# Performance work log

Hardware: AMD Instinct MI355X
Metric: run time of the kernel (lower is better)

The kernel has to match this reference:

```python
import jax, jax.numpy as jnp
import numpy as np

N, E, B = 80000, 480000, 800  # nodes, edges, graphs
H, C = 4, 64                  # attention heads, per-head channels

def gelu(x):
    return jax.nn.gelu(x, approximate=False)

def setup_inputs() -> dict:
    key = jax.random.key(0)
    ks = jax.random.split(key, 40)
    nrm = lambda k, shp, s=0.1: jax.random.normal(k, shp, jnp.float32) * s
    inp = {
        'x': jax.random.normal(ks[0], (N, 21), jnp.float32),
        'edge_index': jax.random.randint(ks[1], (2, E), 0, N, dtype=jnp.int32),
        'batch_idx': jnp.sort(jax.random.randint(ks[2], (N,), 0, B, dtype=jnp.int32)),
        'rnafm': jax.random.normal(ks[3], (B, 640), jnp.float32),
        'hand_feat': jax.random.normal(ks[4], (B, 40), jnp.float32),
        # GATConv params: lin weight [H*C, in], att_src/att_dst [H, C], bias [C]
        'g1_W': nrm(ks[5], (H * C, 21)), 'g1_as': nrm(ks[6], (H, C)), 'g1_ad': nrm(ks[7], (H, C)), 'g1_b': nrm(ks[8], (C,)),
        'g2_W': nrm(ks[9], (H * C, C)), 'g2_as': nrm(ks[10], (H, C)), 'g2_ad': nrm(ks[11], (H, C)), 'g2_b': nrm(ks[12], (C,)),
        'g3_W': nrm(ks[13], (H * C, C)), 'g3_as': nrm(ks[14], (H, C)), 'g3_ad': nrm(ks[15], (H, C)), 'g3_b': nrm(ks[16], (C,)),
        'pool_W': nrm(ks[17], (1, C)), 'pool_b': nrm(ks[18], (1,)),
        'e1_W': nrm(ks[19], (256, 744)), 'e1_b': nrm(ks[20], (256,)),
        'ln_g': jnp.ones((256,), jnp.float32), 'ln_b': jnp.zeros((256,), jnp.float32),
        'e2_W': nrm(ks[21], (128, 256)), 'e2_b': nrm(ks[22], (128,)),
        'bin_W': nrm(ks[23], (1, 128)), 'bin_b': nrm(ks[24], (1,)),
        'ad1_W': nrm(ks[25], (5, 32, 128)), 'ad1_b': nrm(ks[26], (5, 32)),
        'ad2_W': nrm(ks[27], (5, 1, 32)), 'ad2_b': nrm(ks[28], (5, 1)),
        'c1_W': nrm(ks[29], (64, 128)), 'c1_b': nrm(ks[30], (64,)),
        'c2_W': nrm(ks[31], (6, 64)), 'c2_b': nrm(ks[32], (6,)),
    }
    return inp


def reference(x, edge_index, batch_idx, rnafm, hand_feat,
              g1_W, g1_as, g1_ad, g1_b,
              g2_W, g2_as, g2_ad, g2_b,
              g3_W, g3_as, g3_ad, g3_b,
              pool_W, pool_b, e1_W, e1_b, ln_g, ln_b, e2_W, e2_b,
              bin_W, bin_b, ad1_W, ad1_b, ad2_W, ad2_b, c1_W, c1_b, c2_W, c2_b):
    n = x.shape[0]
    # PyG GATConv default: add self loops
    loops = jnp.arange(n, dtype=edge_index.dtype)
    ei = jnp.concatenate([edge_index, jnp.stack([loops, loops])], axis=1)
    src, dst = ei[0], ei[1]

    def gat(h_in, W, a_s, a_d, b):
        h = (h_in @ W.T).reshape(n, H, C)              # [N,H,C]
        s = (h * a_s[None]).sum(-1)                    # [N,H] att_src . h
        d = (h * a_d[None]).sum(-1)                    # [N,H]
        e = jax.nn.leaky_relu(s[src] + d[dst], 0.2)    # [E',H]
        m = jax.ops.segment_max(e, dst, num_segments=n)
        ex = jnp.exp(e - m[dst])                       # segment softmax (stable)
        z = jax.ops.segment_sum(ex, dst, num_segments=n)
        alpha = ex / z[dst]                            # [E',H]
        out = jax.ops.segment_sum(h[src] * alpha[:, :, None], dst, num_segments=n)
        return out.mean(axis=1) + b                    # concat=False -> mean heads

    h = gelu(gat(x, g1_W, g1_as, g1_ad, g1_b))
    h = gelu(gat(h, g2_W, g2_as, g2_ad, g2_b))
    h = gelu(gat(h, g3_W, g3_as, g3_ad, g3_b))

    # attention-weighted pooling; softmax over ALL nodes (dim=0), as in source
    attn = jax.nn.softmax(h @ pool_W.T + pool_b, axis=0)   # [N,1]
    pooled = jax.ops.segment_sum(h * attn, batch_idx, num_segments=B)  # [B,64]

    fused = jnp.concatenate([pooled, rnafm, hand_feat], axis=-1)       # [B,744]
    z1 = gelu(fused @ e1_W.T + e1_b)
    mu = z1.mean(-1, keepdims=True)
    var = ((z1 - mu) ** 2).mean(-1, keepdims=True)
    z1 = (z1 - mu) / jnp.sqrt(var + 1e-5) * ln_g + ln_b
    shared = gelu(z1 @ e2_W.T + e2_b)                      # [B,128]

    binary = (shared @ bin_W.T + bin_b)[:, 0]              # [B]
    h1 = gelu(jnp.einsum('bd,ehd->ebh', shared, ad1_W) + ad1_b[:, None, :])
    per = jnp.einsum('ebh,eh->eb', h1, ad2_W[:, 0, :]) + ad2_b  # [5,B]
    cls = gelu(shared @ c1_W.T + c1_b) @ c2_W.T + c2_b     # [B,6]
    return binary, per, cls
```

## Files before the change

kernel.cpp:

```cpp
#include <hip/hip_runtime.h>
#include <hip/hip_bf16.h>
#include <math.h>

constexpr int N_NODES = 80000;
constexpr int N_EDGES = 480000;
constexpr int N_B     = 800;
constexpr int PADDEG  = 64;

typedef __attribute__((ext_vector_type(8))) short bf16x8;
typedef __attribute__((ext_vector_type(4))) float f32x4;

__device__ __forceinline__ float gelu_exact(float x) {
    return 0.5f * x * (1.0f + erff(x * 0.70710678118654752f));
}
__device__ __forceinline__ float lrelu(float v) {
    return v > 0.f ? v : 0.2f * v;
}
__device__ __forceinline__ unsigned short f2bf(float f) {
    unsigned u = __float_as_uint(f);
    unsigned r = u + 0x7FFFu + ((u >> 16) & 1u);
    return (unsigned short)(r >> 16);
}
__device__ __forceinline__ float bf2f(unsigned short h) {
    return __uint_as_float(((unsigned)h) << 16);
}

template<int IN_DIM>
__launch_bounds__(256, 2)
__global__ void gat_transform(const float* __restrict__ xin,
                              const float* __restrict__ W,
                              const float* __restrict__ aS,
                              const float* __restrict__ aD,
                              unsigned short* __restrict__ hfull,
                              float* __restrict__ sArr,
                              float* __restrict__ dArr) {
    constexpr int K  = (IN_DIM + 31) & ~31;
    constexpr int KS = K / 32;
    constexpr int KP = K + 8;
    __shared__ __align__(16) unsigned short Wb[256 * KP];
    __shared__ __align__(16) unsigned short xs[32 * KP];

    const int tid = threadIdx.x;
    const int lane = tid & 63, w = tid >> 6;

    for (int idx = tid; idx < 256 * K; idx += 256) {
        int c = idx / K, k = idx - c * K;
        Wb[c * KP + k] = (k < IN_DIM) ? f2bf(W[c * IN_DIM + k]) : (unsigned short)0;
    }
    __syncthreads();

    bf16x8 bfrag[4][KS];
    float asv[4], adv[4];
#pragma unroll
    for (int t = 0; t < 4; ++t) {
        const int ch = w * 64 + t * 16 + (lane & 15);
#pragma unroll
        for (int s = 0; s < KS; ++s)
            bfrag[t][s] = *reinterpret_cast<const bf16x8*>(&Wb[ch * KP + s * 32 + (lane >> 4) * 8]);
        asv[t] = aS[ch];
        adv[t] = aD[ch];
    }

    const int ntiles = N_NODES / 32;
    for (int tile = blockIdx.x; tile < ntiles; tile += gridDim.x) {
        const int n0 = tile * 32;
        __syncthreads();
        for (int idx = tid; idx < 32 * K; idx += 256) {
            int r = idx / K, k = idx - r * K;
            xs[r * KP + k] = (k < IN_DIM) ? f2bf(xin[(size_t)(n0 + r) * IN_DIM + k])
                                          : (unsigned short)0;
        }
        __syncthreads();

        f32x4 acc[2][4];
#pragma unroll
        for (int m = 0; m < 2; ++m) {
            bf16x8 afrag[KS];
#pragma unroll
            for (int s = 0; s < KS; ++s)
                afrag[s] = *reinterpret_cast<const bf16x8*>(
                    &xs[(m * 16 + (lane & 15)) * KP + s * 32 + (lane >> 4) * 8]);
#pragma unroll
            for (int t = 0; t < 4; ++t) {
                f32x4 a = {0.f, 0.f, 0.f, 0.f};
#pragma unroll
                for (int s = 0; s < KS; ++s)
                    a = __builtin_amdgcn_mfma_f32_16x16x32_bf16(afrag[s], bfrag[t][s], a, 0, 0, 0);
                acc[m][t] = a;
            }
        }

#pragma unroll
        for (int m = 0; m < 2; ++m) {
            float sv[4] = {0, 0, 0, 0}, dv[4] = {0, 0, 0, 0};
#pragma unroll
            for (int t = 0; t < 4; ++t) {
                const int ch = w * 64 + t * 16 + (lane & 15);
#pragma unroll
                for (int j = 0; j < 4; ++j) {
                    float hv = acc[m][t][j];
                    int node = n0 + m * 16 + (lane >> 4) * 4 + j;
                    hfull[(size_t)node * 256 + ch] = f2bf(hv);
                    sv[j] += hv * asv[t];
                    dv[j] += hv * adv[t];
                }
            }
#pragma unroll
            for (int j = 0; j < 4; ++j) {
                sv[j] += __shfl_xor(sv[j], 1, 64); dv[j] += __shfl_xor(dv[j], 1, 64);
                sv[j] += __shfl_xor(sv[j], 2, 64); dv[j] += __shfl_xor(dv[j], 2, 64);
                sv[j] += __shfl_xor(sv[j], 4, 64); dv[j] += __shfl_xor(dv[j], 4, 64);
                sv[j] += __shfl_xor(sv[j], 8, 64); dv[j] += __shfl_xor(dv[j], 8, 64);
                if ((lane & 15) == 0) {
                    int node = n0 + m * 16 + (lane >> 4) * 4 + j;
                    sArr[node * 4 + w] = sv[j];
                    dArr[node * 4 + w] = dv[j];
                }
            }
        }
    }
}

__global__ void csr_scatter_pad(const int* __restrict__ ei,
                                int* __restrict__ cnt, int* __restrict__ csrc) {
    int e = blockIdx.x * 256 + threadIdx.x;
    if (e >= N_EDGES) return;
    int src = ei[e], dst = ei[N_EDGES + e];
    int slot = atomicAdd(&cnt[dst], 1);
    csrc[(size_t)dst * PADDEG + slot] = src;
}

template<bool POOL>
__launch_bounds__(256)
__global__ void gat_gather(const int* __restrict__ cnt, const int* __restrict__ csrc,
                           const float* __restrict__ sArr, const float* __restrict__ dArr,
                           const unsigned short* __restrict__ hfull,
                           const float* __restrict__ bias,
                           const float* __restrict__ poolW, const float* __restrict__ poolB,
                           float* __restrict__ xout,
                           float* __restrict__ logit, float* __restrict__ pmax) {
    constexpr int CAP = PADDEG;
    __shared__ float qbuf[4][2][CAP * 4];
    __shared__ int   sbuf[4][2][CAP];
    __shared__ float xbuf[4][2][64];
    __shared__ float red[8];

    const int wid = threadIdx.x >> 6;
    const int lane = threadIdx.x & 63;
    const int nl = lane >> 5;
    const int sub = lane & 31;
    const int n = blockIdx.x * 8 + wid * 2 + nl;

    const int jb = n * PADDEG;
    const int deg = cnt[n];

    const int hh = sub & 3;
    const int slot = sub >> 2;
    const float dv = dArr[n * 4 + hh];
    const float lself = lrelu(sArr[n * 4 + hh] + dv);
    float m = lself;

    for (int base = 0; base < deg; base += 8) {
        int s = base + slot;
        float lg = -INFINITY;
        if (s < deg) {
            int src = csrc[jb + s];
            lg = lrelu(sArr[src * 4 + hh] + dv);
            qbuf[wid][nl][s * 4 + hh] = lg;
            if (hh == 0) sbuf[wid][nl][s] = src;
        }
        m = fmaxf(m, lg);
    }
    m = fmaxf(m, __shfl_xor(m, 4, 64));
    m = fmaxf(m, __shfl_xor(m, 8, 64));
    m = fmaxf(m, __shfl_xor(m, 16, 64));
    __threadfence_block();

    float zp = 0.f;
    for (int base = 0; base < deg; base += 8) {
        int s = base + slot;
        if (s < deg) {
            float q = expf(qbuf[wid][nl][s * 4 + hh] - m);
            qbuf[wid][nl][s * 4 + hh] = q;
            zp += q;
        }
    }
    const float qself = expf(lself - m);
    zp += __shfl_xor(zp, 4, 64);
    zp += __shfl_xor(zp, 8, 64);
    zp += __shfl_xor(zp, 16, 64);
    const float inv = 0.25f / (zp + qself);
    __threadfence_block();

    const int h = sub >> 3;
    const int c8 = sub * 8;
    const int bl = (lane & 32) + h;
    const float inv_g = __shfl(inv, bl, 64);
    const float qs_g  = __shfl(qself, bl, 64);

#define LOADU4(S) (*reinterpret_cast<const uint4*>(&hfull[(size_t)(unsigned)(S) * 256 + c8]))
#define UNPK_FMA(A, Q, U) { \
    A[0] = fmaf((Q), __uint_as_float((U).x << 16),          A[0]); \
    A[1] = fmaf((Q), __uint_as_float((U).x & 0xFFFF0000u),  A[1]); \
    A[2] = fmaf((Q), __uint_as_float((U).y << 16),          A[2]); \
    A[3] = fmaf((Q), __uint_as_float((U).y & 0xFFFF0000u),  A[3]); \
    A[4] = fmaf((Q), __uint_as_float((U).z << 16),          A[4]); \
    A[5] = fmaf((Q), __uint_as_float((U).z & 0xFFFF0000u),  A[5]); \
    A[6] = fmaf((Q), __uint_as_float((U).w << 16),          A[6]); \
    A[7] = fmaf((Q), __uint_as_float((U).w & 0xFFFF0000u),  A[7]); }

    float accA[8] = {0, 0, 0, 0, 0, 0, 0, 0};
    float accB[8] = {0, 0, 0, 0, 0, 0, 0, 0};
    {
        uint4 us = LOADU4(n);
        UNPK_FMA(accA, qs_g, us);
    }
    int s = 0;
    for (; s + 1 < deg; s += 2) {
        int s0 = sbuf[wid][nl][s], s1 = sbuf[wid][nl][s + 1];
        float q0 = qbuf[wid][nl][s * 4 + h];
        float q1 = qbuf[wid][nl][(s + 1) * 4 + h];
        uint4 u0 = LOADU4(s0);
        uint4 u1 = LOADU4(s1);
        UNPK_FMA(accA, q0, u0);
        UNPK_FMA(accB, q1, u1);
    }
    if (s < deg) {
        int s0 = sbuf[wid][nl][s];
        float q0 = qbuf[wid][nl][s * 4 + h];
        uint4 u0 = LOADU4(s0);
        UNPK_FMA(accA, q0, u0);
    }
#undef UNPK_FMA
#undef LOADU4

    float acc[8];
#pragma unroll
    for (int j = 0; j < 8; ++j) acc[j] = (accA[j] + accB[j]) * inv_g;

#pragma unroll
    for (int j = 0; j < 8; ++j) {
        acc[j] += __shfl_xor(acc[j], 8, 64);
        acc[j] += __shfl_xor(acc[j], 16, 64);
    }

    {
        float w0 = (h == 0) ? acc[0] : (h == 1) ? acc[2] : (h == 2) ? acc[4] : acc[6];
        float w1 = (h == 0) ? acc[1] : (h == 1) ? acc[3] : (h == 2) ? acc[5] : acc[7];
        const int rc = (sub & 7) * 8 + h * 2;
        xbuf[wid][nl][rc]     = w0;
        xbuf[wid][nl][rc + 1] = w1;
    }
    __threadfence_block();

    const int c2 = sub * 2;
    float o0 = gelu_exact(xbuf[wid][nl][c2]     + bias[c2]);
    float o1 = gelu_exact(xbuf[wid][nl][c2 + 1] + bias[c2 + 1]);
    *reinterpret_cast<float2*>(&xout[(size_t)n * 64 + c2]) = make_float2(o0, o1);

    if (POOL) {
        float p = o0 * poolW[c2] + o1 * poolW[c2 + 1];
#pragma unroll
        for (int of = 1; of < 32; of <<= 1) p += __shfl_xor(p, of, 64);
        float lg = p + poolB[0];
        if (sub == 0) {
            logit[n] = lg;
            red[wid * 2 + nl] = lg;
        }
        __syncthreads();
        if (threadIdx.x == 0) {
            float mm = red[0];
#pragma unroll
            for (int i = 1; i < 8; ++i) mm = fmaxf(mm, red[i]);
            pmax[blockIdx.x] = mm;
        }
    }
}

__global__ void reduce_max(const float* __restrict__ pmax, int n,
                           float* __restrict__ gmax) {
    __shared__ float red[256];
    float m = -INFINITY;
    for (int i = threadIdx.x; i < n; i += 256) m = fmaxf(m, pmax[i]);
    red[threadIdx.x] = m;
    __syncthreads();
    for (int s = 128; s > 0; s >>= 1) {
        if (threadIdx.x < s) red[threadIdx.x] = fmaxf(red[threadIdx.x], red[threadIdx.x + s]);
        __syncthreads();
    }
    if (threadIdx.x == 0) *gmax = red[0];
}

__global__ void seg_bounds(const int* __restrict__ batch, int* __restrict__ start) {
    int n = blockIdx.x * 256 + threadIdx.x;
    if (n >= N_NODES) return;
    int b1 = batch[n];
    int b0 = (n == 0) ? -1 : batch[n - 1];
    for (int b = b0 + 1; b <= b1; ++b) start[b] = n;
    if (n == N_NODES - 1)
        for (int b = b1 + 1; b <= N_B; ++b) start[b] = N_NODES;
}

__global__ void pool_graph(const float* __restrict__ h3,
                           const float* __restrict__ logit,
                           const float* __restrict__ gmax,
                           const int* __restrict__ start,
                           float* __restrict__ pooled,
                           float* __restrict__ gsum) {
    __shared__ float sacc[4][64];
    __shared__ float sw[4];
    int b = blockIdx.x;
    int s = start[b], e = start[b + 1];
    int lane = threadIdx.x & 63, wid = threadIdx.x >> 6;
    float M = *gmax;
    float acc = 0.f, wsum = 0.f;
    for (int n = s + wid; n < e; n += 4) {
        float w = expf(logit[n] - M);
        acc += h3[(size_t)n * 64 + lane] * w;
        if (lane == 0) wsum += w;
    }
    sacc[wid][lane] = acc;
    if (lane == 0) sw[wid] = wsum;
    __syncthreads();
    if (wid == 0) {
        pooled[(size_t)b * 64 + lane] = sacc[0][lane] + sacc[1][lane] + sacc[2][lane] + sacc[3][lane];
        if (lane == 0) atomicAdd(gsum, sw[0] + sw[1] + sw[2] + sw[3]);
    }
}

constexpr int GB1  = 8;
constexpr int KSEG = 372;

__launch_bounds__(256, 4)
__global__ void head1_part(const float* __restrict__ pooled, const float* __restrict__ gsum,
                           const float* __restrict__ rnafm, const float* __restrict__ hand,
                           const float* __restrict__ e1W,
                           float* __restrict__ part) {
    __shared__ __align__(16) float fused[GB1][KSEG + 4];
    const int bq = blockIdx.x >> 1;
    const int ks = blockIdx.x & 1;
    const int g0 = bq * GB1;
    const int k0 = ks * KSEG;
    const int tid = threadIdx.x;
    const float inv = 1.0f / *gsum;

    for (int idx = tid; idx < GB1 * KSEG; idx += 256) {
        int g = idx / KSEG, kk = idx - g * KSEG;
        int k = kk + k0;
        int b = g0 + g;
        float v;
        if (k < 64)       v = pooled[(size_t)b * 64 + k] * inv;
        else if (k < 704) v = rnafm[(size_t)b * 640 + (k - 64)];
        else              v = hand[(size_t)b * 40 + (k - 704)];
        fused[g][kk] = v;
    }
    __syncthreads();

    const float* wr = e1W + (size_t)tid * 744 + k0;
    float a0 = 0.f, a1 = 0.f, a2 = 0.f, a3 = 0.f;
    float a4 = 0.f, a5 = 0.f, a6 = 0.f, a7 = 0.f;
    for (int q = 0; q < KSEG / 4; ++q) {
        float4 w4 = *reinterpret_cast<const float4*>(wr + q * 4);
        float4 f0 = *reinterpret_cast<const float4*>(&fused[0][q * 4]);
        float4 f1 = *reinterpret_cast<const float4*>(&fused[1][q * 4]);
        float4 f2 = *reinterpret_cast<const float4*>(&fused[2][q * 4]);
        float4 f3 = *reinterpret_cast<const float4*>(&fused[3][q * 4]);
        float4 f4 = *reinterpret_cast<const float4*>(&fused[4][q * 4]);
        float4 f5 = *reinterpret_cast<const float4*>(&fused[5][q * 4]);
        float4 f6 = *reinterpret_cast<const float4*>(&fused[6][q * 4]);
        float4 f7 = *reinterpret_cast<const float4*>(&fused[7][q * 4]);
        a0 += f0.x * w4.x + f0.y * w4.y + f0.z * w4.z + f0.w * w4.w;
        a1 += f1.x * w4.x + f1.y * w4.y + f1.z * w4.z + f1.w * w4.w;
        a2 += f2.x * w4.x + f2.y * w4.y + f2.z * w4.z + f2.w * w4.w;
        a3 += f3.x * w4.x + f3.y * w4.y + f3.z * w4.z + f3.w * w4.w;
        a4 += f4.x * w4.x + f4.y * w4.y + f4.z * w4.z + f4.w * w4.w;
        a5 += f5.x * w4.x + f5.y * w4.y + f5.z * w4.z + f5.w * w4.w;
        a6 += f6.x * w4.x + f6.y * w4.y + f6.z * w4.z + f6.w * w4.w;
        a7 += f7.x * w4.x + f7.y * w4.y + f7.z * w4.z + f7.w * w4.w;
    }
    float* po = part + ((size_t)ks * N_B + g0) * 256 + tid;
    po[0 * 256] = a0; po[1 * 256] = a1; po[2 * 256] = a2; po[3 * 256] = a3;
    po[4 * 256] = a4; po[5 * 256] = a5; po[6 * 256] = a6; po[7 * 256] = a7;
}

__launch_bounds__(256, 4)
__global__ void head1_fin(const float* __restrict__ part,
                          const float* __restrict__ e1b,
                          const float* __restrict__ lng, const float* __restrict__ lnb,
                          float* __restrict__ z1) {
    __shared__ float red1[4][4], red2[4][4];
    const int b0 = blockIdx.x * 4;
    const int tid = threadIdx.x;
    const int lane = tid & 63, wid = tid >> 6;
    const float eb = e1b[tid];

    float g0, g1, g2, g3;
    {
        float v0 = part[(size_t)(b0 + 0) * 256 + tid] + part[((size_t)N_B + b0 + 0) * 256 + tid] + eb;
        float v1 = part[(size_t)(b0 + 1) * 256 + tid] + part[((size_t)N_B + b0 + 1) * 256 + tid] + eb;
        float v2 = part[(size_t)(b0 + 2) * 256 + tid] + part[((size_t)N_B + b0 + 2) * 256 + tid] + eb;
        float v3 = part[(size_t)(b0 + 3) * 256 + tid] + part[((size_t)N_B + b0 + 3) * 256 + tid] + eb;
        g0 = gelu_exact(v0); g1 = gelu_exact(v1); g2 = gelu_exact(v2); g3 = gelu_exact(v3);
    }

    float s10 = g0, s11 = g1, s12 = g2, s13 = g3;
    float s20 = g0 * g0, s21 = g1 * g1, s22 = g2 * g2, s23 = g3 * g3;
#pragma unroll
    for (int o = 1; o < 64; o <<= 1) {
        s10 += __shfl_xor(s10, o, 64); s11 += __shfl_xor(s11, o, 64);
        s12 += __shfl_xor(s12, o, 64); s13 += __shfl_xor(s13, o, 64);
        s20 += __shfl_xor(s20, o, 64); s21 += __shfl_xor(s21, o, 64);
        s22 += __shfl_xor(s22, o, 64); s23 += __shfl_xor(s23, o, 64);
    }
    if (lane == 0) {
        red1[wid][0] = s10; red1[wid][1] = s11; red1[wid][2] = s12; red1[wid][3] = s13;
        red2[wid][0] = s20; red2[wid][1] = s21; red2[wid][2] = s22; red2[wid][3] = s23;
    }
    __syncthreads();

    const float gN = lng[tid], bN = lnb[tid];
#pragma unroll
    for (int bb = 0; bb < 4; ++bb) {
        float s1 = red1[0][bb] + red1[1][bb] + red1[2][bb] + red1[3][bb];
        float s2 = red2[0][bb] + red2[1][bb] + red2[2][bb] + red2[3][bb];
        float mu  = s1 * (1.0f / 256.0f);
        float var = s2 * (1.0f / 256.0f) - mu * mu;
        float g = (bb == 0) ? g0 : (bb == 1) ? g1 : (bb == 2) ? g2 : g3;
        z1[(size_t)(b0 + bb) * 256 + tid] = (g - mu) * rsqrtf(var + 1e-5f) * gN + bN;
    }
}

__launch_bounds__(128, 8)
__global__ void head2(const float* __restrict__ z1,
                      const float* __restrict__ e2W, const float* __restrict__ e2b,
                      float* __restrict__ shr) {
    __shared__ float zr[4][256];
    const int b0 = blockIdx.x * 4;
    const int tid = threadIdx.x;
    for (int bb = 0; bb < 4; ++bb)
        for (int k = tid; k < 256; k += 128)
            zr[bb][k] = z1[(size_t)(b0 + bb) * 256 + k];
    __syncthreads();

    const float* wr = e2W + (size_t)tid * 256;
    const float eb = e2b[tid];
    float acc0 = eb, acc1 = eb, acc2 = eb, acc3 = eb;
    for (int k = 0; k < 256; k += 4) {
        float4 w4 = *reinterpret_cast<const float4*>(wr + k);
        float4 f0 = *reinterpret_cast<const float4*>(&zr[0][k]);
        float4 f1 = *reinterpret_cast<const float4*>(&zr[1][k]);
        float4 f2 = *reinterpret_cast<const float4*>(&zr[2][k]);
        float4 f3 = *reinterpret_cast<const float4*>(&zr[3][k]);
        acc0 += f0.x * w4.x + f0.y * w4.y + f0.z * w4.z + f0.w * w4.w;
        acc1 += f1.x * w4.x + f1.y * w4.y + f1.z * w4.z + f1.w * w4.w;
        acc2 += f2.x * w4.x + f2.y * w4.y + f2.z * w4.z + f2.w * w4.w;
        acc3 += f3.x * w4.x + f3.y * w4.y + f3.z * w4.z + f3.w * w4.w;
    }
    shr[(size_t)(b0 + 0) * 128 + tid] = gelu_exact(acc0);
    shr[(size_t)(b0 + 1) * 128 + tid] = gelu_exact(acc1);
    shr[(size_t)(b0 + 2) * 128 + tid] = gelu_exact(acc2);
    shr[(size_t)(b0 + 3) * 128 + tid] = gelu_exact(acc3);
}

__global__ void head3(const float* __restrict__ shr,
                      const float* __restrict__ binW, const float* __restrict__ binB,
                      const float* __restrict__ ad1W, const float* __restrict__ ad1b,
                      const float* __restrict__ ad2W, const float* __restrict__ ad2b,
                      const float* __restrict__ c1W, const float* __restrict__ c1b,
                      const float* __restrict__ c2W, const float* __restrict__ c2b,
                      float* __restrict__ out) {
    __shared__ float sv[128];
    __shared__ float t64[64];
    __shared__ float h1s[5][32];
    int b = blockIdx.x, tid = threadIdx.x;
    if (tid < 128) sv[tid] = shr[(size_t)b * 128 + tid];
    __syncthreads();
    if (tid == 0) {
        float a = binB[0];
        for (int k = 0; k < 128; ++k) a += sv[k] * binW[k];
        out[b] = a;
    }
    if (tid < 64) {
        float a = c1b[tid];
        const float* wr = c1W + (size_t)tid * 128;
        for (int k = 0; k < 128; ++k) a += sv[k] * wr[k];
        t64[tid] = gelu_exact(a);
    }
    if (tid >= 64 && tid < 224) {
        int idx = tid - 64, e = idx >> 5, hh = idx & 31;
        float a = ad1b[e * 32 + hh];
        const float* wr = ad1W + (size_t)(e * 32 + hh) * 128;
        for (int k = 0; k < 128; ++k) a += sv[k] * wr[k];
        h1s[e][hh] = gelu_exact(a);
    }
    __syncthreads();
    if (tid < 6) {
        float a = c2b[tid];
        const float* wr = c2W + (size_t)tid * 64;
        for (int k = 0; k < 64; ++k) a += t64[k] * wr[k];
        out[4800 + (size_t)b * 6 + tid] = a;
    }
    if (tid >= 8 && tid < 13) {
        int e = tid - 8;
        float a = ad2b[e];
        const float* wr = ad2W + (size_t)e * 32;
        for (int k = 0; k < 32; ++k) a += h1s[e][k] * wr[k];
        out[800 + (size_t)e * 800 + b] = a;
    }
}

extern "C" void kernel_launch(void* const* d_in, const int* in_sizes, int n_in,
                              void* d_out, int out_size, void* d_ws, size_t ws_size,
                              hipStream_t stream) {
    const float* x       = (const float*)d_in[0];
    const int*   ei      = (const int*)d_in[1];
    const int*   batch   = (const int*)d_in[2];
    const float* rnafm   = (const float*)d_in[3];
    const float* hand    = (const float*)d_in[4];
    const float* gW[3]  = {(const float*)d_in[5],  (const float*)d_in[9],  (const float*)d_in[13]};
    const float* gAs[3] = {(const float*)d_in[6],  (const float*)d_in[10], (const float*)d_in[14]};
    const float* gAd[3] = {(const float*)d_in[7],  (const float*)d_in[11], (const float*)d_in[15]};
    const float* gB[3]  = {(const float*)d_in[8],  (const float*)d_in[12], (const float*)d_in[16]};
    const float* poolW = (const float*)d_in[17];
    const float* poolB = (const float*)d_in[18];
    const float* e1W = (const float*)d_in[19]; const float* e1b = (const float*)d_in[20];
    const float* lng = (const float*)d_in[21]; const float* lnb = (const float*)d_in[22];
    const float* e2W = (const float*)d_in[23]; const float* e2b = (const float*)d_in[24];
    const float* binW = (const float*)d_in[25]; const float* binB = (const float*)d_in[26];
    const float* ad1W = (const float*)d_in[27]; const float* ad1b = (const float*)d_in[28];
    const float* ad2W = (const float*)d_in[29]; const float* ad2b = (const float*)d_in[30];
    const float* c1W = (const float*)d_in[31]; const float* c1b = (const float*)d_in[32];
    const float* c2W = (const float*)d_in[33]; const float* c2b = (const float*)d_in[34];
    float* out = (float*)d_out;

    float* ws = (float*)d_ws;
    size_t off = 0;
    unsigned short* hfull = (unsigned short*)(ws + off); off += (size_t)N_NODES * 128;
    float* xcur   = ws + off; off += (size_t)N_NODES * 64;
    float* sArr   = ws + off; off += (size_t)N_NODES * 4;
    float* dArr   = ws + off; off += (size_t)N_NODES * 4;
    int*   cnt    = (int*)(ws + off); off += N_NODES;
    int*   csrc   = (int*)(ws + off); off += (size_t)N_NODES * PADDEG;
    float* logit  = ws + off; off += N_NODES;
    float* pmax   = ws + off; off += 20000;
    float* pooled = ws + off; off += (size_t)N_B * 64;
    float* part   = ws + off; off += (size_t)2 * N_B * 256;
    float* z1     = ws + off; off += (size_t)N_B * 256;
    float* shr    = ws + off; off += (size_t)N_B * 128;
    int*   start  = (int*)(ws + off); off += (N_B + 1);
    float* gmax   = ws + off; off += 1;
    float* gsum   = ws + off; off += 1;

    hipMemsetAsync(cnt, 0, N_NODES * sizeof(int), stream);
    csr_scatter_pad<<<(N_EDGES + 255) / 256, 256, 0, stream>>>(ei, cnt, csrc);
    seg_bounds<<<(N_NODES + 255) / 256, 256, 0, stream>>>(batch, start);

    for (int layer = 0; layer < 3; ++layer) {
        const float* xin = (layer == 0) ? x : xcur;
        if (layer == 0)
            gat_transform<21><<<512, 256, 0, stream>>>(xin, gW[0], gAs[0], gAd[0], hfull, sArr, dArr);
        else
            gat_transform<64><<<512, 256, 0, stream>>>(xin, gW[layer], gAs[layer], gAd[layer], hfull, sArr, dArr);
        if (layer < 2)
            gat_gather<false><<<N_NODES / 8, 256, 0, stream>>>(cnt, csrc, sArr, dArr, hfull,
                                                               gB[layer], nullptr, nullptr,
                                                               xcur, nullptr, nullptr);
        else
            gat_gather<true><<<N_NODES / 8, 256, 0, stream>>>(cnt, csrc, sArr, dArr, hfull,
                                                              gB[2], poolW, poolB,
                                                              xcur, logit, pmax);
    }

    reduce_max<<<1, 256, 0, stream>>>(pmax, N_NODES / 8, gmax);
    hipMemsetAsync(gsum, 0, sizeof(float), stream);
    pool_graph<<<N_B, 256, 0, stream>>>(xcur, logit, gmax, start, pooled, gsum);

    head1_part<<<(N_B / GB1) * 2, 256, 0, stream>>>(pooled, gsum, rnafm, hand, e1W, part);
    head1_fin<<<N_B / 4, 256, 0, stream>>>(part, e1b, lng, lnb, z1);
    head2<<<N_B / 4, 128, 0, stream>>>(z1, e2W, e2b, shr);
    head3<<<N_B, 256, 0, stream>>>(shr, binW, binB, ad1W, ad1b, ad2W, ad2b, c1W, c1b, c2W, c2b, out);
}
```

Measured before the change: 367.0 us.

## Fuse MLP head kernels into one and unroll gather loop by four

Merges the three head kernels (layernorm finish, e2 projection, output heads) into one kernel that keeps intermediates in shared memory, processing four graphs per block. This drops two launches and the global round-trips for z1 and the shared features. It also unrolls the GAT neighbour gather by four with a vector index load, to put more independent memory loads in flight. The fused kernel runs fewer blocks with a larger shared-memory footprint, and the head3 work per graph is now spread over fewer threads.

```diff
diff --git a/kernel.cpp b/kernel.cpp
--- a/kernel.cpp
+++ b/kernel.cpp
@@ -216,6 +216,21 @@
         UNPK_FMA(accA, qs_g, us);
     }
     int s = 0;
+    for (; s + 3 < deg; s += 4) {
+        int4 sv4 = *reinterpret_cast<const int4*>(&sbuf[wid][nl][s]);
+        float q0 = qbuf[wid][nl][(s + 0) * 4 + h];
+        float q1 = qbuf[wid][nl][(s + 1) * 4 + h];
+        float q2 = qbuf[wid][nl][(s + 2) * 4 + h];
+        float q3 = qbuf[wid][nl][(s + 3) * 4 + h];
+        uint4 u0 = LOADU4(sv4.x);
+        uint4 u1 = LOADU4(sv4.y);
+        uint4 u2 = LOADU4(sv4.z);
+        uint4 u3 = LOADU4(sv4.w);
+        UNPK_FMA(accA, q0, u0);
+        UNPK_FMA(accB, q1, u1);
+        UNPK_FMA(accA, q2, u2);
+        UNPK_FMA(accB, q3, u3);
+    }
     for (; s + 1 < deg; s += 2) {
         int s0 = sbuf[wid][nl][s], s1 = sbuf[wid][nl][s + 1];
         float q0 = qbuf[wid][nl][s * 4 + h];
@@ -383,25 +398,32 @@
     po[4 * 256] = a4; po[5 * 256] = a5; po[6 * 256] = a6; po[7 * 256] = a7;
 }
 
-__launch_bounds__(256, 4)
-__global__ void head1_fin(const float* __restrict__ part,
-                          const float* __restrict__ e1b,
-                          const float* __restrict__ lng, const float* __restrict__ lnb,
-                          float* __restrict__ z1) {
+__launch_bounds__(256, 2)
+__global__ void head_fused(const float* __restrict__ part,
+                           const float* __restrict__ e1b,
+                           const float* __restrict__ lng, const float* __restrict__ lnb,
+                           const float* __restrict__ e2W, const float* __restrict__ e2b,
+                           const float* __restrict__ binW, const float* __restrict__ binB,
+                           const float* __restrict__ ad1W, const float* __restrict__ ad1b,
+                           const float* __restrict__ ad2W, const float* __restrict__ ad2b,
+                           const float* __restrict__ c1W, const float* __restrict__ c1b,
+                           const float* __restrict__ c2W, const float* __restrict__ c2b,
+                           float* __restrict__ out) {
+    __shared__ float zr[4][256];
     __shared__ float red1[4][4], red2[4][4];
+    __shared__ float sv[4][128];
+    __shared__ float t64[4][64];
+    __shared__ float h1s[4][5][32];
+    __shared__ float binred[4][32];
     const int b0 = blockIdx.x * 4;
     const int tid = threadIdx.x;
     const int lane = tid & 63, wid = tid >> 6;
+
     const float eb = e1b[tid];
-
-    float g0, g1, g2, g3;
-    {
-        float v0 = part[(size_t)(b0 + 0) * 256 + tid] + part[((size_t)N_B + b0 + 0) * 256 + tid] + eb;
-        float v1 = part[(size_t)(b0 + 1) * 256 + tid] + part[((size_t)N_B + b0 + 1) * 256 + tid] + eb;
-        float v2 = part[(size_t)(b0 + 2) * 256 + tid] + part[((size_t)N_B + b0 + 2) * 256 + tid] + eb;
-        float v3 = part[(size_t)(b0 + 3) * 256 + tid] + part[((size_t)N_B + b0 + 3) * 256 + tid] + eb;
-        g0 = gelu_exact(v0); g1 = gelu_exact(v1); g2 = gelu_exact(v2); g3 = gelu_exact(v3);
-    }
+    float g0 = gelu_exact(part[(size_t)(b0 + 0) * 256 + tid] + part[((size_t)N_B + b0 + 0) * 256 + tid] + eb);
+    float g1 = gelu_exact(part[(size_t)(b0 + 1) * 256 + tid] + part[((size_t)N_B + b0 + 1) * 256 + tid] + eb);
+    float g2 = gelu_exact(part[(size_t)(b0 + 2) * 256 + tid] + part[((size_t)N_B + b0 + 2) * 256 + tid] + eb);
+    float g3 = gelu_exact(part[(size_t)(b0 + 3) * 256 + tid] + part[((size_t)N_B + b0 + 3) * 256 + tid] + eb);
 
     float s10 = g0, s11 = g1, s12 = g2, s13 = g3;
     float s20 = g0 * g0, s21 = g1 * g1, s22 = g2 * g2, s23 = g3 * g3;
@@ -426,86 +448,73 @@
         float mu  = s1 * (1.0f / 256.0f);
         float var = s2 * (1.0f / 256.0f) - mu * mu;
         float g = (bb == 0) ? g0 : (bb == 1) ? g1 : (bb == 2) ? g2 : g3;
-        z1[(size_t)(b0 + bb) * 256 + tid] = (g - mu) * rsqrtf(var + 1e-5f) * gN + bN;
-    }
-}
-
-__launch_bounds__(128, 8)
-__global__ void head2(const float* __restrict__ z1,
-                      const float* __restrict__ e2W, const float* __restrict__ e2b,
-                      float* __restrict__ shr) {
-    __shared__ float zr[4][256];
-    const int b0 = blockIdx.x * 4;
-    const int tid = threadIdx.x;
-    for (int bb = 0; bb < 4; ++bb)
-        for (int k = tid; k < 256; k += 128)
-            zr[bb][k] = z1[(size_t)(b0 + bb) * 256 + k];
-    __syncthreads();
-
-    const float* wr = e2W + (size_t)tid * 256;
-    const float eb = e2b[tid];
-    float acc0 = eb, acc1 = eb, acc2 = eb, acc3 = eb;
-    for (int k = 0; k < 256; k += 4) {
-        float4 w4 = *reinterpret_cast<const float4*>(wr + k);
-        float4 f0 = *reinterpret_cast<const float4*>(&zr[0][k]);
-        float4 f1 = *reinterpret_cast<const float4*>(&zr[1][k]);
-        float4 f2 = *reinterpret_cast<const float4*>(&zr[2][k]);
-        float4 f3 = *reinterpret_cast<const float4*>(&zr[3][k]);
-        acc0 += f0.x * w4.x + f0.y * w4.y + f0.z * w4.z + f0.w * w4.w;
-        acc1 += f1.x * w4.x + f1.y * w4.y + f1.z * w4.z + f1.w * w4.w;
-        acc2 += f2.x * w4.x + f2.y * w4.y + f2.z * w4.z + f2.w * w4.w;
-        acc3 += f3.x * w4.x + f3.y * w4.y + f3.z * w4.z + f3.w * w4.w;
-    }
-    shr[(size_t)(b0 + 0) * 128 + tid] = gelu_exact(acc0);
-    shr[(size_t)(b0 + 1) * 128 + tid] = gelu_exact(acc1);
-    shr[(size_t)(b0 + 2) * 128 + tid] = gelu_exact(acc2);
-    shr[(size_t)(b0 + 3) * 128 + tid] = gelu_exact(acc3);
-}
-
-__global__ void head3(const float* __restrict__ shr,
-                      const float* __restrict__ binW, const float* __restrict__ binB,
-                      const float* __restrict__ ad1W, const float* __restrict__ ad1b,
-                      const float* __restrict__ ad2W, const float* __restrict__ ad2b,
-                      const float* __restrict__ c1W, const float* __restrict__ c1b,
-                      const float* __restrict__ c2W, const float* __restrict__ c2b,
-                      float* __restrict__ out) {
-    __shared__ float sv[128];
-    __shared__ float t64[64];
-    __shared__ float h1s[5][32];
-    int b = blockIdx.x, tid = threadIdx.x;
-    if (tid < 128) sv[tid] = shr[(size_t)b * 128 + tid];
-    __syncthreads();
-    if (tid == 0) {
-        float a = binB[0];
-        for (int k = 0; k < 128; ++k) a += sv[k] * binW[k];
-        out[b] = a;
-    }
-    if (tid < 64) {
-        float a = c1b[tid];
-        const float* wr = c1W + (size_t)tid * 128;
-        for (int k = 0; k < 128; ++k) a += sv[k] * wr[k];
-        t64[tid] = gelu_exact(a);
-    }
-    if (tid >= 64 && tid < 224) {
-        int idx = tid - 64, e = idx >> 5, hh = idx & 31;
-        float a = ad1b[e * 32 + hh];
-        const float* wr = ad1W + (size_t)(e * 32 + hh) * 128;
-        for (int k = 0; k < 128; ++k) a += sv[k] * wr[k];
-        h1s[e][hh] = gelu_exact(a);
-    }
-    __syncthreads();
-    if (tid < 6) {
-        float a = c2b[tid];
-        const float* wr = c2W + (size_t)tid * 64;
-        for (int k = 0; k < 64; ++k) a += t64[k] * wr[k];
-        out[4800 + (size_t)b * 6 + tid] = a;
-    }
-    if (tid >= 8 && tid < 13) {
-        int e = tid - 8;
+        zr[bb][tid] = (g - mu) * rsqrtf(var + 1e-5f) * gN + bN;
+    }
+    __syncthreads();
+
+    {
+        const int ch = tid & 127, gp = tid >> 7;
+        const float* wr = e2W + (size_t)ch * 256;
+        const float e2bb = e2b[ch];
+        float a0 = e2bb, a1 = e2bb;
+        for (int k = 0; k < 256; k += 4) {
+            float4 w4 = *reinterpret_cast<const float4*>(wr + k);
+            float4 f0 = *reinterpret_cast<const float4*>(&zr[gp * 2][k]);
+            float4 f1 = *reinterpret_cast<const float4*>(&zr[gp * 2 + 1][k]);
+            a0 += f0.x * w4.x + f0.y * w4.y + f0.z * w4.z + f0.w * w4.w;
+            a1 += f1.x * w4.x + f1.y * w4.y + f1.z * w4.z + f1.w * w4.w;
+        }
+        sv[gp * 2][ch]     = gelu_exact(a0);
+        sv[gp * 2 + 1][ch] = gelu_exact(a1);
+    }
+    __syncthreads();
+
+    for (int idx = tid; idx < 256 + 640; idx += 256) {
+        if (idx < 256) {
+            int g = idx >> 6, ch = idx & 63;
+            float a = c1b[ch];
+            const float* wr = c1W + (size_t)ch * 128;
+            for (int k = 0; k < 128; ++k) a += sv[g][k] * wr[k];
+            t64[g][ch] = gelu_exact(a);
+        } else {
+            int j = idx - 256;
+            int g = j / 160, r = j - g * 160;
+            int e = r >> 5, hh = r & 31;
+            float a = ad1b[e * 32 + hh];
+            const float* wr = ad1W + (size_t)(e * 32 + hh) * 128;
+            for (int k = 0; k < 128; ++k) a += sv[g][k] * wr[k];
+            h1s[g][e][hh] = gelu_exact(a);
+        }
+    }
+    if (tid < 128) {
+        int g = tid >> 5, r = tid & 31;
+        float a = 0.f;
+#pragma unroll
+        for (int k = 0; k < 4; ++k) a += sv[g][r * 4 + k] * binW[r * 4 + k];
+        binred[g][r] = a;
+    }
+    __syncthreads();
+
+    if (tid < 24) {
+        int g = tid / 6, c = tid - g * 6;
+        float a = c2b[c];
+        const float* wr = c2W + (size_t)c * 64;
+        for (int k = 0; k < 64; ++k) a += t64[g][k] * wr[k];
+        out[4800 + (size_t)(b0 + g) * 6 + c] = a;
+    }
+    if (tid >= 32 && tid < 52) {
+        int j = tid - 32;
+        int g = j / 5, e = j - g * 5;
         float a = ad2b[e];
         const float* wr = ad2W + (size_t)e * 32;
-        for (int k = 0; k < 32; ++k) a += h1s[e][k] * wr[k];
-        out[800 + (size_t)e * 800 + b] = a;
+        for (int k = 0; k < 32; ++k) a += h1s[g][e][k] * wr[k];
+        out[800 + (size_t)e * 800 + (b0 + g)] = a;
+    }
+    if (tid >= 64 && tid < 68) {
+        int g = tid - 64;
+        float a = binB[0];
+        for (int r = 0; r < 32; ++r) a += binred[g][r];
+        out[b0 + g] = a;
     }
 }
 
@@ -545,8 +554,6 @@
     float* pmax   = ws + off; off += 20000;
     float* pooled = ws + off; off += (size_t)N_B * 64;
     float* part   = ws + off; off += (size_t)2 * N_B * 256;
-    float* z1     = ws + off; off += (size_t)N_B * 256;
-    float* shr    = ws + off; off += (size_t)N_B * 128;
     int*   start  = (int*)(ws + off); off += (N_B + 1);
     float* gmax   = ws + off; off += 1;
     float* gsum   = ws + off; off += 1;
@@ -576,7 +583,7 @@
     pool_graph<<<N_B, 256, 0, stream>>>(xcur, logit, gmax, start, pooled, gsum);
 
     head1_part<<<(N_B / GB1) * 2, 256, 0, stream>>>(pooled, gsum, rnafm, hand, e1W, part);
-    head1_fin<<<N_B / 4, 256, 0, stream>>>(part, e1b, lng, lnb, z1);
-    head2<<<N_B / 4, 128, 0, stream>>>(z1, e2W, e2b, shr);
-    head3<<<N_B, 256, 0, stream>>>(shr, binW, binB, ad1W, ad1b, ad2W, ad2b, c1W, c1b, c2W, c2b, out);
-}
+    head_fused<<<N_B / 4, 256, 0, stream>>>(part, e1b, lng, lnb, e2W, e2b,
+                                            binW, binB, ad1W, ad1b, ad2W, ad2b,
+                                            c1W, c1b, c2W, c2b, out);
+}
```

Result: no change. 364.2 us (-0.7%).
